# Performance work log

Measured on AMD Instinct MI355X. Metric: run time of the kernel, lower is better.

The kernel has to match this reference:

```python
import jax, jax.numpy as jnp
import numpy as np

THRESHOLD = 0.05

def binarize101(w, threshold):
    # Ternary quantization to {-1, 0, +1}: zero inside the dead-zone [-thr, thr].
    pos = (w > threshold).astype(w.dtype)
    neg = (w < -threshold).astype(w.dtype)
    return pos - neg

def setup_inputs() -> dict:
    key = jax.random.key(0)
    k1, k2, k3 = jax.random.split(key, 3)
    x = jax.random.normal(k1, (8192, 4096), dtype=jnp.float32)
    weight = jax.random.normal(k2, (4096, 4096), dtype=jnp.float32)
    bias = jax.random.normal(k3, (4096,), dtype=jnp.float32)
    return {"x": x, "weight": weight, "bias": bias}

def reference(x, weight, bias):
    wb = binarize101(weight, THRESHOLD)
    # F.linear: x @ wb.T + bias ; x: [N, in], weight: [out, in] -> [N, out]
    return jnp.einsum('ni,oi->no', x, wb) + bias
```

## Files before the change

kernel.cpp:

```cpp
#include <hip/hip_runtime.h>

typedef float floatx4 __attribute__((ext_vector_type(4)));
typedef __bf16 bf16x8 __attribute__((ext_vector_type(8)));
using u16 = unsigned short;
using u32 = unsigned int;

#define GLOBAL_AS __attribute__((address_space(1)))
#define LDS_AS    __attribute__((address_space(3)))

__global__ void cvt_x_kernel(const float* __restrict__ x, u16* __restrict__ xb, int n8) {
  int stride = gridDim.x * blockDim.x;
  for (int i = blockIdx.x * blockDim.x + threadIdx.x; i < n8; i += stride) {
    const float4* p = (const float4*)(x + (size_t)i * 8);
    float4 a = p[0], b = p[1];
    float v[8] = {a.x, a.y, a.z, a.w, b.x, b.y, b.z, b.w};
    u32 r[8];
#pragma unroll
    for (int j = 0; j < 8; ++j) {
      u32 u = __float_as_uint(v[j]);
      r[j] = (u + 0x7FFFu + ((u >> 16) & 1u)) >> 16;
    }
    uint4 o;
    o.x = r[0] | (r[1] << 16);
    o.y = r[2] | (r[3] << 16);
    o.z = r[4] | (r[5] << 16);
    o.w = r[6] | (r[7] << 16);
    *(uint4*)(xb + (size_t)i * 8) = o;
  }
}

__global__ void quant_w_kernel(const float* __restrict__ w, u16* __restrict__ wb, int n8) {
  int stride = gridDim.x * blockDim.x;
  for (int i = blockIdx.x * blockDim.x + threadIdx.x; i < n8; i += stride) {
    const float4* p = (const float4*)(w + (size_t)i * 8);
    float4 a = p[0], b = p[1];
    float v[8] = {a.x, a.y, a.z, a.w, b.x, b.y, b.z, b.w};
    u32 r[8];
#pragma unroll
    for (int j = 0; j < 8; ++j) {
      r[j] = (v[j] > 0.05f) ? 0x3F80u : ((v[j] < -0.05f) ? -1.0f == -1.0f ? 0xBF80u : 0u : 0u);
    }
    uint4 o;
    o.x = r[0] | (r[1] << 16);
    o.y = r[2] | (r[3] << 16);
    o.z = r[4] | (r[5] << 16);
    o.w = r[6] | (r[7] << 16);
    *(uint4*)(wb + (size_t)i * 8) = o;
  }
}

__global__ __launch_bounds__(512, 2) void gemm_bin_pipe(
    const u16* __restrict__ A, const u16* __restrict__ B,
    const float* __restrict__ bias, float* __restrict__ C,
    int M, int N, int K) {
  __shared__ u16 lds[65536];

  const int tid = threadIdx.x;
  const int w = tid >> 6, l = tid & 63;
  const int wr = w >> 2, wc = w & 3;
  const int r = l & 15;

  const int nbn = N >> 8;
  int wg = blockIdx.x;
  const int nwg = gridDim.x;
  if ((nwg & 7) == 0) wg = (wg & 7) * (nwg >> 3) + (wg >> 3);
  const int bm = wg / nbn, bn = wg % nbn;

  const int NSTEPS = K >> 5;

  const int prow = ((tid >> 6) << 4) + (tid & 15);
  const int pk = ((tid >> 4) & 3) << 3;
  const size_t Abase = (size_t)(bm * 256 + prow) * K + pk;
  const size_t Bbase = (size_t)(bn * 256 + prow) * K + pk;
  const size_t chunkStride = (size_t)128 * K;

  const u16* const ldsA = lds + wr * 4096 + l * 8;
  const u16* const ldsB = lds + 8192 + wc * 2048 + l * 8;

  floatx4 acc[8][4] = {};
  bf16x8 afA[8], bfA[4], afB[8], bfB[4];

#define GLOAD(gptr, ldsoff)                                                    \
  __builtin_amdgcn_global_load_lds((const GLOBAL_AS void*)(gptr),              \
                                   (LDS_AS void*)(lds + (ldsoff)), 16, 0, 0)

  for (int u = 0; u < 4; ++u) {
    const int so = u * 16384;
    const u16* ga = A + Abase + (size_t)u * 32;
    const u16* gb = B + Bbase + (size_t)u * 32;
    GLOAD(ga, so + tid * 8);
    GLOAD(ga + chunkStride, so + 4096 + tid * 8);
    GLOAD(gb, so + 8192 + tid * 8);
    GLOAD(gb + chunkStride, so + 12288 + tid * 8);
  }
  asm volatile("s_waitcnt vmcnt(8)" ::: "memory");
  __builtin_amdgcn_s_barrier();
#pragma unroll
  for (int m = 0; m < 8; ++m) afA[m] = *(const bf16x8*)(ldsA + m * 512);
#pragma unroll
  for (int n = 0; n < 4; ++n) bfA[n] = *(const bf16x8*)(ldsB + n * 512);

#define STEP(s, CURA, CURB, NXTA, NXTB)                                        \
  {                                                                            \
    if ((s) >= 1 && (s) + 3 < NSTEPS) {                                        \
      const int sd_ = (((s) + 3) & 3) * 16384;                                 \
      const u16* ga_ = A + Abase + (size_t)((s) + 3) * 32;                     \
      const u16* gb_ = B + Bbase + (size_t)((s) + 3) * 32;                     \
      GLOAD(ga_, sd_ + tid * 8);                                               \
      GLOAD(ga_ + chunkStride, sd_ + 4096 + tid * 8);                          \
      GLOAD(gb_, sd_ + 8192 + tid * 8);                                        \
      GLOAD(gb_ + chunkStride, sd_ + 12288 + tid * 8);                         \
    }                                                                          \
    const int son_ = (((s) + 1) & 3) * 16384;                                  \
    _Pragma("unroll")                                                          \
    for (int m = 0; m < 8; ++m) NXTA[m] = *(const bf16x8*)(ldsA + son_ + m * 512); \
    _Pragma("unroll")                                                          \
    for (int n = 0; n < 4; ++n) NXTB[n] = *(const bf16x8*)(ldsB + son_ + n * 512); \
    asm volatile("s_waitcnt lgkmcnt(12)" ::: "memory");                        \
    __builtin_amdgcn_sched_barrier(0);                                         \
    __builtin_amdgcn_s_setprio(1);                                             \
    _Pragma("unroll")                                                          \
    for (int m = 0; m < 8; ++m)                                                \
      _Pragma("unroll")                                                        \
      for (int n = 0; n < 4; ++n)                                              \
        acc[m][n] = __builtin_amdgcn_mfma_f32_16x16x32_bf16(CURA[m], CURB[n],  \
                                                            acc[m][n], 0, 0, 0); \
    __builtin_amdgcn_s_setprio(0);                                             \
    __builtin_amdgcn_sched_barrier(0);                                         \
    if ((s) + 1 < NSTEPS) {                                                    \
      if ((s) + 3 < NSTEPS) asm volatile("s_waitcnt vmcnt(4)" ::: "memory");   \
      else                  asm volatile("s_waitcnt vmcnt(0)" ::: "memory");   \
      __builtin_amdgcn_s_barrier();                                            \
    }                                                                          \
  }

  for (int t = 0; t < (NSTEPS >> 1); ++t) {
    const int s0 = t << 1;
    STEP(s0,     afA, bfA, afB, bfB);
    STEP(s0 + 1, afB, bfB, afA, bfA);
  }
#undef STEP
#undef GLOAD

  const int g = l >> 4;
  const int colb = bn * 256 + wc * 64;
  float bv[4];
#pragma unroll
  for (int n = 0; n < 4; ++n) bv[n] = bias[colb + n * 16 + r];
  const int rowb0 = bm * 256 + wr * 128;
#pragma unroll
  for (int m = 0; m < 8; ++m) {
    const int rowb = rowb0 + m * 16 + g * 4;
#pragma unroll
    for (int n = 0; n < 4; ++n) {
      const int col = colb + n * 16 + r;
      float* cp = C + (size_t)rowb * N + col;
#pragma unroll
      for (int q = 0; q < 4; ++q) cp[(size_t)q * N] = acc[m][n][q] + bv[n];
    }
  }
}

__global__ void gemm_naive_kernel(const float* __restrict__ x, const float* __restrict__ wgt,
                                  const float* __restrict__ bias, float* __restrict__ out,
                                  int M, int N, int K) {
  long long idx = (long long)blockIdx.x * blockDim.x + threadIdx.x;
  if (idx >= (long long)M * N) return;
  int o = (int)(idx % N);
  int m = (int)(idx / N);
  const float* xr = x + (size_t)m * K;
  const float* wr = wgt + (size_t)o * K;
  float s = 0.f;
  for (int i = 0; i < K; ++i) {
    float wv = wr[i];
    float t = (wv > 0.05f) ? 1.f : ((wv < -0.05f) ? -1.f : 0.f);
    s = fmaf(xr[i], t, s);
  }
  out[idx] = s + bias[o];
}

extern "C" void kernel_launch(void* const* d_in, const int* in_sizes, int n_in,
                              void* d_out, int out_size, void* d_ws, size_t ws_size,
                              hipStream_t stream) {
  const float* x    = (const float*)d_in[0];
  const float* wgt  = (const float*)d_in[1];
  const float* bias = (const float*)d_in[2];
  float* out = (float*)d_out;

  const int N = in_sizes[2];
  const int K = in_sizes[1] / N;
  const int M = in_sizes[0] / K;

  const size_t need = ((size_t)M * K + (size_t)N * K) * sizeof(u16);
  if (ws_size >= need && (M % 256 == 0) && (N % 256 == 0) && (K % 64 == 0) && K >= 256) {
    u16* xb = (u16*)d_ws;
    u16* wb = xb + (size_t)M * K;
    const int nx8 = (M * K) / 8;
    const int nw8 = (N * K) / 8;
    cvt_x_kernel<<<2048, 256, 0, stream>>>(x, xb, nx8);
    quant_w_kernel<<<2048, 256, 0, stream>>>(wgt, wb, nw8);
    const int grid = (M / 256) * (N / 256);
    gemm_bin_pipe<<<grid, 512, 0, stream>>>(xb, wb, bias, out, M, N, K);
  } else {
    const long long total = (long long)M * N;
    gemm_naive_kernel<<<(unsigned)((total + 255) / 256), 256, 0, stream>>>(x, wgt, bias, out, M, N, K);
  }
}
```

Measured before the change: 326.7 us.

## Pre-permute ternary weights into fragment order and load B directly to registers

The weight quantization kernel now writes the bf16 ternary weights in a layout that matches the MFMA fragment order per 256-column tile. The GEMM reads B straight from global memory into registers, keeps only A in LDS (halved LDS, double-buffered with a 64-wide K tile), and splits each tile's MFMAs into quarters with two A fragment reloads. This removes B's LDS traffic and barriers, at the cost of exposed global-load latency on B. Waiting for lgkmcnt(0) before each MFMA batch also reduces overlap.

```diff
diff --git a/kernel.cpp b/kernel.cpp
--- a/kernel.cpp
+++ b/kernel.cpp
@@ -29,31 +29,39 @@
   }
 }
 
-__global__ void quant_w_kernel(const float* __restrict__ w, u16* __restrict__ wb, int n8) {
+__global__ void quant_w_perm(const float* __restrict__ w, u16* __restrict__ wb,
+                             int K, int Kd8, int n8) {
   int stride = gridDim.x * blockDim.x;
   for (int i = blockIdx.x * blockDim.x + threadIdx.x; i < n8; i += stride) {
-    const float4* p = (const float4*)(w + (size_t)i * 8);
+    const int n = i / Kd8;
+    const int k = (i - n * Kd8) * 8;
+    const float4* p = (const float4*)(w + (size_t)n * K + k);
     float4 a = p[0], b = p[1];
     float v[8] = {a.x, a.y, a.z, a.w, b.x, b.y, b.z, b.w};
     u32 r[8];
 #pragma unroll
     for (int j = 0; j < 8; ++j) {
-      r[j] = (v[j] > 0.05f) ? 0x3F80u : ((v[j] < -0.05f) ? -1.0f == -1.0f ? 0xBF80u : 0u : 0u);
+      r[j] = (v[j] > 0.05f) ? 0x3F80u : ((v[j] < -0.05f) ? 0xBF80u : 0u);
     }
     uint4 o;
     o.x = r[0] | (r[1] << 16);
     o.y = r[2] | (r[3] << 16);
     o.z = r[4] | (r[5] << 16);
     o.w = r[6] | (r[7] << 16);
-    *(uint4*)(wb + (size_t)i * 8) = o;
-  }
-}
-
-__global__ __launch_bounds__(512, 2) void gemm_bin_pipe(
-    const u16* __restrict__ A, const u16* __restrict__ B,
+    const int bnp = n >> 8, nl = n & 255;
+    const int wcg = nl >> 6, ng = (nl >> 4) & 3, rr = nl & 15;
+    const int tile = k >> 6, jj = (k >> 5) & 1, g = (k >> 3) & 3;
+    const int f = ng * 2 + jj, l = g * 16 + rr;
+    u16* dst = wb + (size_t)bnp * 256 * K + tile * 16384 + wcg * 4096 + f * 512 + l * 8;
+    *(uint4*)dst = o;
+  }
+}
+
+__global__ __launch_bounds__(512, 2) void gemm_bdir(
+    const u16* __restrict__ A, const u16* __restrict__ Bp,
     const float* __restrict__ bias, float* __restrict__ C,
     int M, int N, int K) {
-  __shared__ u16 lds[65536];
+  __shared__ u16 lds[32768];
 
   const int tid = threadIdx.x;
   const int w = tid >> 6, l = tid & 63;
@@ -66,81 +74,98 @@
   if ((nwg & 7) == 0) wg = (wg & 7) * (nwg >> 3) + (wg >> 3);
   const int bm = wg / nbn, bn = wg % nbn;
 
-  const int NSTEPS = K >> 5;
-
-  const int prow = ((tid >> 6) << 4) + (tid & 15);
-  const int pk = ((tid >> 4) & 3) << 3;
-  const size_t Abase = (size_t)(bm * 256 + prow) * K + pk;
-  const size_t Bbase = (size_t)(bn * 256 + prow) * K + pk;
-  const size_t chunkStride = (size_t)128 * K;
-
-  const u16* const ldsA = lds + wr * 4096 + l * 8;
-  const u16* const ldsB = lds + 8192 + wc * 2048 + l * 8;
+  const int T = K >> 6;
+
+  const u16* Asrc[4];
+#pragma unroll
+  for (int c = 0; c < 4; ++c) {
+    const int e = c * 4096 + tid * 8;
+    const int half = e >> 13, fi = (e >> 9) & 15, ll = (e >> 3) & 63;
+    const int mg = fi >> 1, j = fi & 1, g = ll >> 4, rr2 = ll & 15;
+    const int row = bm * 256 + half * 128 + mg * 16 + rr2;
+    Asrc[c] = A + (size_t)row * K + j * 32 + g * 8;
+  }
+  const u16* const Bbase = Bp + (size_t)bn * 256 * K + wc * 4096 + l * 8;
+  const u16* const ldsA = lds + wr * 8192 + l * 8;
 
   floatx4 acc[8][4] = {};
-  bf16x8 afA[8], bfA[4], afB[8], bfB[4];
-
-#define GLOAD(gptr, ldsoff)                                                    \
-  __builtin_amdgcn_global_load_lds((const GLOBAL_AS void*)(gptr),              \
-                                   (LDS_AS void*)(lds + (ldsoff)), 16, 0, 0)
-
-  for (int u = 0; u < 4; ++u) {
-    const int so = u * 16384;
-    const u16* ga = A + Abase + (size_t)u * 32;
-    const u16* gb = B + Bbase + (size_t)u * 32;
-    GLOAD(ga, so + tid * 8);
-    GLOAD(ga + chunkStride, so + 4096 + tid * 8);
-    GLOAD(gb, so + 8192 + tid * 8);
-    GLOAD(gb + chunkStride, so + 12288 + tid * 8);
-  }
+  bf16x8 af[8], BAs[8], BBs[8];
+
+#define AST(tt, bufoff)                                                        \
+  {                                                                            \
+    _Pragma("unroll")                                                          \
+    for (int c = 0; c < 4; ++c)                                                \
+      __builtin_amdgcn_global_load_lds(                                        \
+          (const GLOBAL_AS void*)(Asrc[c] + (size_t)(tt) * 64),                \
+          (LDS_AS void*)(lds + (bufoff) + c * 4096 + tid * 8), 16, 0, 0);      \
+  }
+#define BLD(tt, DST)                                                           \
+  {                                                                            \
+    _Pragma("unroll")                                                          \
+    for (int f = 0; f < 8; ++f)                                                \
+      DST[f] = *(const bf16x8*)(Bbase + (size_t)(tt) * 16384 + f * 512);       \
+  }
+
+  AST(0, 0);
+  BLD(0, BAs);
   asm volatile("s_waitcnt vmcnt(8)" ::: "memory");
   __builtin_amdgcn_s_barrier();
-#pragma unroll
-  for (int m = 0; m < 8; ++m) afA[m] = *(const bf16x8*)(ldsA + m * 512);
-#pragma unroll
-  for (int n = 0; n < 4; ++n) bfA[n] = *(const bf16x8*)(ldsB + n * 512);
-
-#define STEP(s, CURA, CURB, NXTA, NXTB)                                        \
+
+#define MFMA_Q(MGOFF, NGOFF, CUR)                                              \
+  __builtin_amdgcn_s_setprio(1);                                               \
+  _Pragma("unroll")                                                            \
+  for (int mg = 0; mg < 4; ++mg)                                               \
+    _Pragma("unroll")                                                          \
+    for (int ng = 0; ng < 2; ++ng)                                             \
+      _Pragma("unroll")                                                        \
+      for (int j = 0; j < 2; ++j)                                              \
+        acc[(MGOFF) + mg][(NGOFF) + ng] =                                      \
+            __builtin_amdgcn_mfma_f32_16x16x32_bf16(                           \
+                af[mg * 2 + j], CUR[(NGOFF) * 2 + ng * 2 + j],                 \
+                acc[(MGOFF) + mg][(NGOFF) + ng], 0, 0, 0);                     \
+  __builtin_amdgcn_s_setprio(0);
+
+#define TILE(t, CUR, NXT, DOST)                                                \
   {                                                                            \
-    if ((s) >= 1 && (s) + 3 < NSTEPS) {                                        \
-      const int sd_ = (((s) + 3) & 3) * 16384;                                 \
-      const u16* ga_ = A + Abase + (size_t)((s) + 3) * 32;                     \
-      const u16* gb_ = B + Bbase + (size_t)((s) + 3) * 32;                     \
-      GLOAD(ga_, sd_ + tid * 8);                                               \
-      GLOAD(ga_ + chunkStride, sd_ + 4096 + tid * 8);                          \
-      GLOAD(gb_, sd_ + 8192 + tid * 8);                                        \
-      GLOAD(gb_ + chunkStride, sd_ + 12288 + tid * 8);                         \
+    const int buf_ = ((t) & 1) * 16384;                                        \
+    if (DOST) {                                                                \
+      AST((t) + 1, buf_ ^ 16384);                                              \
+      BLD((t) + 1, NXT);                                                       \
     }                                                                          \
-    const int son_ = (((s) + 1) & 3) * 16384;                                  \
-    _Pragma("unroll")                                                          \
-    for (int m = 0; m < 8; ++m) NXTA[m] = *(const bf16x8*)(ldsA + son_ + m * 512); \
-    _Pragma("unroll")                                                          \
-    for (int n = 0; n < 4; ++n) NXTB[n] = *(const bf16x8*)(ldsB + son_ + n * 512); \
-    asm volatile("s_waitcnt lgkmcnt(12)" ::: "memory");                        \
+                                                   \
+    _Pragma("unroll")                                                          \
+    for (int fi = 0; fi < 8; ++fi)                                             \
+      af[fi] = *(const bf16x8*)(ldsA + buf_ + fi * 512);                       \
+    asm volatile("s_waitcnt lgkmcnt(0)" ::: "memory");                         \
     __builtin_amdgcn_sched_barrier(0);                                         \
-    __builtin_amdgcn_s_setprio(1);                                             \
-    _Pragma("unroll")                                                          \
-    for (int m = 0; m < 8; ++m)                                                \
-      _Pragma("unroll")                                                        \
-      for (int n = 0; n < 4; ++n)                                              \
-        acc[m][n] = __builtin_amdgcn_mfma_f32_16x16x32_bf16(CURA[m], CURB[n],  \
-                                                            acc[m][n], 0, 0, 0); \
-    __builtin_amdgcn_s_setprio(0);                                             \
+    MFMA_Q(0, 0, CUR)                                                          \
+                                                                       \
+    MFMA_Q(0, 2, CUR)                                                          \
+                                                  \
+    _Pragma("unroll")                                                          \
+    for (int fi = 0; fi < 8; ++fi)                                             \
+      af[fi] = *(const bf16x8*)(ldsA + buf_ + 4096 + fi * 512);                \
+    asm volatile("s_waitcnt lgkmcnt(0)" ::: "memory");                         \
     __builtin_amdgcn_sched_barrier(0);                                         \
-    if ((s) + 1 < NSTEPS) {                                                    \
-      if ((s) + 3 < NSTEPS) asm volatile("s_waitcnt vmcnt(4)" ::: "memory");   \
-      else                  asm volatile("s_waitcnt vmcnt(0)" ::: "memory");   \
+    MFMA_Q(4, 0, CUR)                                                          \
+                                                                       \
+    MFMA_Q(4, 2, CUR)                                                          \
+    if (DOST) {                                                                \
+      asm volatile("s_waitcnt vmcnt(8)" ::: "memory");  \
       __builtin_amdgcn_s_barrier();                                            \
     }                                                                          \
   }
 
-  for (int t = 0; t < (NSTEPS >> 1); ++t) {
-    const int s0 = t << 1;
-    STEP(s0,     afA, bfA, afB, bfB);
-    STEP(s0 + 1, afB, bfB, afA, bfA);
-  }
-#undef STEP
-#undef GLOAD
+  for (int t2 = 0; t2 < T - 2; t2 += 2) {
+    TILE(t2,     BAs, BBs, true);
+    TILE(t2 + 1, BBs, BAs, true);
+  }
+  TILE(T - 2, BAs, BBs, true);
+  TILE(T - 1, BBs, BAs, false);
+#undef TILE
+#undef MFMA_Q
+#undef AST
+#undef BLD
 
   const int g = l >> 4;
   const int colb = bn * 256 + wc * 64;
@@ -198,9 +223,9 @@
     const int nx8 = (M * K) / 8;
     const int nw8 = (N * K) / 8;
     cvt_x_kernel<<<2048, 256, 0, stream>>>(x, xb, nx8);
-    quant_w_kernel<<<2048, 256, 0, stream>>>(wgt, wb, nw8);
+    quant_w_perm<<<2048, 256, 0, stream>>>(wgt, wb, K, K / 8, nw8);
     const int grid = (M / 256) * (N / 256);
-    gemm_bin_pipe<<<grid, 512, 0, stream>>>(xb, wb, bias, out, M, N, K);
+    gemm_bdir<<<grid, 512, 0, stream>>>(xb, wb, bias, out, M, N, K);
   } else {
     const long long total = (long long)M * N;
     gemm_naive_kernel<<<(unsigned)((total + 255) / 256), 256, 0, stream>>>(x, wgt, bias, out, M, N, K);
```

After: 366.0 us. +12.1%, slower.

## Pack ternary weights to 2 bits and decode into LDS inside GEMM

Applied to the files above, without the earlier changes.

Weights are quantized into a 2-bit-per-element packed format, pre-swizzled into the per-tile LDS fragment order, so the GEMM reads one-eighth the B bytes of the bf16 version. The GEMM decodes the packed codes to bf16 in registers and writes them to LDS. It also switches to 64-wide K tiles with double buffering and splits each tile into four MFMA quarter-phases with interleaved loads and barriers. This trades B memory bandwidth and the bf16 weight write for extra ALU decode work, more barriers per tile, and a less deeply pipelined A prefetch.

```diff
diff --git a/kernel.cpp b/kernel.cpp
--- a/kernel.cpp
+++ b/kernel.cpp
@@ -29,28 +29,33 @@
   }
 }
 
-__global__ void quant_w_kernel(const float* __restrict__ w, u16* __restrict__ wb, int n8) {
+__global__ void quant_w_pack(const float* __restrict__ w, u16* __restrict__ wb,
+                             int K, int Kd8, int n8) {
   int stride = gridDim.x * blockDim.x;
   for (int i = blockIdx.x * blockDim.x + threadIdx.x; i < n8; i += stride) {
-    const float4* p = (const float4*)(w + (size_t)i * 8);
+    const int n = i / Kd8;
+    const int k = (i - n * Kd8) * 8;
+    const float4* p = (const float4*)(w + (size_t)n * K + k);
     float4 a = p[0], b = p[1];
     float v[8] = {a.x, a.y, a.z, a.w, b.x, b.y, b.z, b.w};
-    u32 r[8];
-#pragma unroll
-    for (int j = 0; j < 8; ++j) {
-      r[j] = (v[j] > 0.05f) ? 0x3F80u : ((v[j] < -0.05f) ? -1.0f == -1.0f ? 0xBF80u : 0u : 0u);
+    u32 pk = 0;
+#pragma unroll
+    for (int e = 0; e < 8; ++e) {
+      u32 c = (v[e] > 0.05f) ? 1u : ((v[e] < -0.05f) ? 3u : 0u);
+      pk |= c << (2 * e);
     }
-    uint4 o;
-    o.x = r[0] | (r[1] << 16);
-    o.y = r[2] | (r[3] << 16);
-    o.z = r[4] | (r[5] << 16);
-    o.w = r[6] | (r[7] << 16);
-    *(uint4*)(wb + (size_t)i * 8) = o;
-  }
-}
-
-__global__ __launch_bounds__(512, 2) void gemm_bin_pipe(
-    const u16* __restrict__ A, const u16* __restrict__ B,
+    const int panel = n >> 8, nl = n & 255;
+    const int wc = nl >> 6, ng = (nl >> 4) & 3, r = nl & 15;
+    const int tile = k >> 6, j = (k >> 5) & 1, g = (k >> 3) & 3;
+    const int f = ng * 2 + j, l = g * 16 + r;
+    const int wf = ((f >> 2) << 4) + (wc << 2) + (f & 3);
+    const int idx = ((wf >> 2) << 8) + (l << 2) + (wf & 3);
+    wb[(size_t)panel * (K >> 6) * 2048 + tile * 2048 + idx] = (u16)pk;
+  }
+}
+
+__global__ __launch_bounds__(512, 2) void gemm_bin_pk(
+    const u16* __restrict__ A, const u16* __restrict__ Bp,
     const float* __restrict__ bias, float* __restrict__ C,
     int M, int N, int K) {
   __shared__ u16 lds[65536];
@@ -66,81 +71,160 @@
   if ((nwg & 7) == 0) wg = (wg & 7) * (nwg >> 3) + (wg >> 3);
   const int bm = wg / nbn, bn = wg % nbn;
 
-  const int NSTEPS = K >> 5;
-
-  const int prow = ((tid >> 6) << 4) + (tid & 15);
-  const int pk = ((tid >> 4) & 3) << 3;
-  const size_t Abase = (size_t)(bm * 256 + prow) * K + pk;
-  const size_t Bbase = (size_t)(bn * 256 + prow) * K + pk;
-  const size_t chunkStride = (size_t)128 * K;
-
-  const u16* const ldsA = lds + wr * 4096 + l * 8;
-  const u16* const ldsB = lds + 8192 + wc * 2048 + l * 8;
+  const int T = K >> 6;
+
+  const int srow = ((tid >> 7) << 4) + (tid & 15);
+  const int skk = (((tid >> 6) & 1) << 5) + (((tid >> 4) & 3) << 3);
+  const size_t aLo0 = (size_t)(bm * 256 + srow) * K + skk;
+  const size_t cs = (size_t)128 * K;
+
+  const u16* const pkp = Bp + (size_t)bn * (K >> 6) * 2048 + ((tid >> 6) << 8) + ((tid & 63) << 2);
+  const int bdst = 16384 + ((tid >> 6) << 11) + ((tid & 63) << 3);
+
+  const u16* const afp0 = lds + wr * 8192 + l * 8;
+  const u16* const bfp0 = lds + 16384 + wc * 2048 + l * 8;
 
   floatx4 acc[8][4] = {};
-  bf16x8 afA[8], bfA[4], afB[8], bfB[4];
-
-#define GLOAD(gptr, ldsoff)                                                    \
+  bf16x8 af[8], bflo[4], bfhi[4];
+  uint2 pkA, pkB;
+
+#define GLOAD(gptr, u16off)                                                    \
   __builtin_amdgcn_global_load_lds((const GLOBAL_AS void*)(gptr),              \
-                                   (LDS_AS void*)(lds + (ldsoff)), 16, 0, 0)
-
-  for (int u = 0; u < 4; ++u) {
-    const int so = u * 16384;
-    const u16* ga = A + Abase + (size_t)u * 32;
-    const u16* gb = B + Bbase + (size_t)u * 32;
-    GLOAD(ga, so + tid * 8);
-    GLOAD(ga + chunkStride, so + 4096 + tid * 8);
-    GLOAD(gb, so + 8192 + tid * 8);
-    GLOAD(gb + chunkStride, so + 12288 + tid * 8);
-  }
-  asm volatile("s_waitcnt vmcnt(8)" ::: "memory");
-  __builtin_amdgcn_s_barrier();
-#pragma unroll
-  for (int m = 0; m < 8; ++m) afA[m] = *(const bf16x8*)(ldsA + m * 512);
-#pragma unroll
-  for (int n = 0; n < 4; ++n) bfA[n] = *(const bf16x8*)(ldsB + n * 512);
-
-#define STEP(s, CURA, CURB, NXTA, NXTB)                                        \
+                                   (LDS_AS void*)(lds + (u16off)), 16, 0, 0)
+#define BARRIER __builtin_amdgcn_s_barrier()
+#define LGKM0  do { asm volatile("s_waitcnt lgkmcnt(0)" ::: "memory");         \
+                    __builtin_amdgcn_sched_barrier(0); } while (0)
+
+#define DECODE(PK, bufn_)                                                      \
   {                                                                            \
-    if ((s) >= 1 && (s) + 3 < NSTEPS) {                                        \
-      const int sd_ = (((s) + 3) & 3) * 16384;                                 \
-      const u16* ga_ = A + Abase + (size_t)((s) + 3) * 32;                     \
-      const u16* gb_ = B + Bbase + (size_t)((s) + 3) * 32;                     \
-      GLOAD(ga_, sd_ + tid * 8);                                               \
-      GLOAD(ga_ + chunkStride, sd_ + 4096 + tid * 8);                          \
-      GLOAD(gb_, sd_ + 8192 + tid * 8);                                        \
-      GLOAD(gb_ + chunkStride, sd_ + 12288 + tid * 8);                         \
+    _Pragma("unroll")                                                          \
+    for (int q = 0; q < 4; ++q) {                                              \
+      u32 word = (q < 2) ? PK.x : PK.y;                                        \
+      u32 vv = (q & 1) ? (word >> 16) : (word & 0xFFFFu);                      \
+      u32 o[4];                                                                \
+      _Pragma("unroll")                                                        \
+      for (int ii = 0; ii < 4; ++ii) {                                         \
+        u32 x = (vv >> (4 * ii)) & 0xFu;                                       \
+        u32 c0 = x & 3u, c1 = x >> 2;                                          \
+        u32 lo = c0 * 0x3F80u + ((c0 >> 1) << 8);                              \
+        u32 hi = c1 * 0x3F80u + ((c1 >> 1) << 8);                              \
+        o[ii] = lo | (hi << 16);                                               \
+      }                                                                        \
+      uint4 ov; ov.x = o[0]; ov.y = o[1]; ov.z = o[2]; ov.w = o[3];            \
+      *(uint4*)(lds + (bufn_) + bdst + q * 512) = ov;                          \
     }                                                                          \
-    const int son_ = (((s) + 1) & 3) * 16384;                                  \
-    _Pragma("unroll")                                                          \
-    for (int m = 0; m < 8; ++m) NXTA[m] = *(const bf16x8*)(ldsA + son_ + m * 512); \
-    _Pragma("unroll")                                                          \
-    for (int n = 0; n < 4; ++n) NXTB[n] = *(const bf16x8*)(ldsB + son_ + n * 512); \
-    asm volatile("s_waitcnt lgkmcnt(12)" ::: "memory");                        \
-    __builtin_amdgcn_sched_barrier(0);                                         \
-    __builtin_amdgcn_s_setprio(1);                                             \
-    _Pragma("unroll")                                                          \
-    for (int m = 0; m < 8; ++m)                                                \
-      _Pragma("unroll")                                                        \
-      for (int n = 0; n < 4; ++n)                                              \
-        acc[m][n] = __builtin_amdgcn_mfma_f32_16x16x32_bf16(CURA[m], CURB[n],  \
-                                                            acc[m][n], 0, 0, 0); \
-    __builtin_amdgcn_s_setprio(0);                                             \
-    __builtin_amdgcn_sched_barrier(0);                                         \
-    if ((s) + 1 < NSTEPS) {                                                    \
-      if ((s) + 3 < NSTEPS) asm volatile("s_waitcnt vmcnt(4)" ::: "memory");   \
-      else                  asm volatile("s_waitcnt vmcnt(0)" ::: "memory");   \
-      __builtin_amdgcn_s_barrier();                                            \
+  }
+
+  pkA = *(const uint2*)(pkp);
+  pkB = *(const uint2*)(pkp + 2048);
+  GLOAD(A + aLo0,                    0 + tid * 8);
+  GLOAD(A + aLo0 + cs,            8192 + tid * 8);
+  GLOAD(A + aLo0 + (size_t)64 * K,        4096 + tid * 8);
+  GLOAD(A + aLo0 + (size_t)64 * K + cs,  12288 + tid * 8);
+  DECODE(pkA, 0)
+  asm volatile("s_waitcnt vmcnt(0)" ::: "memory");
+  asm volatile("s_waitcnt lgkmcnt(0)" ::: "memory");
+  BARRIER;
+
+#define TILE(t, PKC, PKN)                                                      \
+  {                                                                            \
+    const int bufc = ((t) & 1) << 15;                                          \
+    const int bufn = bufc ^ 32768;                                             \
+    const bool doSt = (t) + 1 < T;                                             \
+    const bool doPk = (t) + 2 < T;                                             \
+    const size_t kadv = (size_t)((t) + 1) << 6;                                \
+    const u16* afp = afp0 + bufc;                                              \
+    const u16* bfp = bfp0 + bufc;                                              \
+            \
+    if (doPk) PKN = *(const uint2*)(pkp + (size_t)((t) + 2) * 2048);           \
+    _Pragma("unroll")                                                          \
+    for (int i = 0; i < 8; ++i) af[i] = *(const bf16x8*)(afp + i * 512);       \
+    _Pragma("unroll")                                                          \
+    for (int i = 0; i < 4; ++i) bflo[i] = *(const bf16x8*)(bfp + i * 512);     \
+    if (doSt) {                                                                \
+      GLOAD(A + aLo0 + kadv,      bufn + 0 + tid * 8);                         \
+      GLOAD(A + aLo0 + cs + kadv, bufn + 8192 + tid * 8);                      \
     }                                                                          \
-  }
-
-  for (int t = 0; t < (NSTEPS >> 1); ++t) {
-    const int s0 = t << 1;
-    STEP(s0,     afA, bfA, afB, bfB);
-    STEP(s0 + 1, afB, bfB, afA, bfA);
-  }
-#undef STEP
+    asm volatile("s_waitcnt lgkmcnt(8)" ::: "memory");                         \
+    BARRIER;                                                                   \
+    LGKM0;                                                                     \
+    __builtin_amdgcn_s_setprio(1);                                             \
+    _Pragma("unroll")                                                          \
+    for (int j = 0; j < 2; ++j)                                                \
+      _Pragma("unroll")                                                        \
+      for (int mg = 0; mg < 4; ++mg)                                           \
+        _Pragma("unroll")                                                      \
+        for (int ng = 0; ng < 2; ++ng)                                         \
+          acc[mg][ng] = __builtin_amdgcn_mfma_f32_16x16x32_bf16(               \
+              af[mg * 2 + j], bflo[ng * 2 + j], acc[mg][ng], 0, 0, 0);         \
+    __builtin_amdgcn_s_setprio(0);                                             \
+    BARRIER;                                                                   \
+                 \
+    _Pragma("unroll")                                                          \
+    for (int i = 0; i < 4; ++i) bfhi[i] = *(const bf16x8*)(bfp + 8192 + i * 512); \
+    if (doSt) DECODE(PKC, bufn)                                                \
+    BARRIER;                                                                   \
+    LGKM0;                                                                     \
+    __builtin_amdgcn_s_setprio(1);                                             \
+    _Pragma("unroll")                                                          \
+    for (int j = 0; j < 2; ++j)                                                \
+      _Pragma("unroll")                                                        \
+      for (int mg = 0; mg < 4; ++mg)                                           \
+        _Pragma("unroll")                                                      \
+        for (int ng = 0; ng < 2; ++ng)                                         \
+          acc[mg][2 + ng] = __builtin_amdgcn_mfma_f32_16x16x32_bf16(           \
+              af[mg * 2 + j], bfhi[ng * 2 + j], acc[mg][2 + ng], 0, 0, 0);     \
+    __builtin_amdgcn_s_setprio(0);                                             \
+    if (doPk) asm volatile("s_waitcnt vmcnt(3)" ::: "memory");                 \
+    else      asm volatile("s_waitcnt vmcnt(0)" ::: "memory");                 \
+    BARRIER;                                                                   \
+                                       \
+    _Pragma("unroll")                                                          \
+    for (int i = 0; i < 8; ++i) af[i] = *(const bf16x8*)(afp + 4096 + i * 512); \
+    asm volatile("s_waitcnt lgkmcnt(4)" ::: "memory");                         \
+    BARRIER;                                                                   \
+    LGKM0;                                                                     \
+    __builtin_amdgcn_s_setprio(1);                                             \
+    _Pragma("unroll")                                                          \
+    for (int j = 0; j < 2; ++j)                                                \
+      _Pragma("unroll")                                                        \
+      for (int mg = 0; mg < 4; ++mg)                                           \
+        _Pragma("unroll")                                                      \
+        for (int ng = 0; ng < 2; ++ng)                                         \
+          acc[4 + mg][ng] = __builtin_amdgcn_mfma_f32_16x16x32_bf16(           \
+              af[mg * 2 + j], bflo[ng * 2 + j], acc[4 + mg][ng], 0, 0, 0);     \
+    __builtin_amdgcn_s_setprio(0);                                             \
+    BARRIER;                                                                   \
+                                     \
+    if (doSt) {                                                                \
+      GLOAD(A + aLo0 + (size_t)64 * K + kadv,      bufn + 4096 + tid * 8);     \
+      GLOAD(A + aLo0 + (size_t)64 * K + cs + kadv, bufn + 12288 + tid * 8);    \
+    }                                                                          \
+    BARRIER;                                                                   \
+    __builtin_amdgcn_s_setprio(1);                                             \
+    _Pragma("unroll")                                                          \
+    for (int j = 0; j < 2; ++j)                                                \
+      _Pragma("unroll")                                                        \
+      for (int mg = 0; mg < 4; ++mg)                                           \
+        _Pragma("unroll")                                                      \
+        for (int ng = 0; ng < 2; ++ng)                                         \
+          acc[4 + mg][2 + ng] = __builtin_amdgcn_mfma_f32_16x16x32_bf16(       \
+              af[mg * 2 + j], bfhi[ng * 2 + j], acc[4 + mg][2 + ng], 0, 0, 0); \
+    __builtin_amdgcn_s_setprio(0);                                             \
+    if (doPk) asm volatile("s_waitcnt vmcnt(2)" ::: "memory");                 \
+    else      asm volatile("s_waitcnt vmcnt(0)" ::: "memory");                 \
+    BARRIER;                                                                   \
+  }
+
+  for (int tt = 0; tt < T; tt += 2) {
+    TILE(tt,     pkB, pkA)
+    TILE(tt + 1, pkA, pkB)
+  }
+#undef TILE
+#undef DECODE
 #undef GLOAD
+#undef BARRIER
+#undef LGKM0
 
   const int g = l >> 4;
   const int colb = bn * 256 + wc * 64;
@@ -191,16 +275,16 @@
   const int K = in_sizes[1] / N;
   const int M = in_sizes[0] / K;
 
-  const size_t need = ((size_t)M * K + (size_t)N * K) * sizeof(u16);
-  if (ws_size >= need && (M % 256 == 0) && (N % 256 == 0) && (K % 64 == 0) && K >= 256) {
+  const size_t need = (size_t)M * K * 2 + (size_t)N * K / 4;
+  if (ws_size >= need && (M % 256 == 0) && (N % 256 == 0) && (K % 128 == 0) && K >= 256) {
     u16* xb = (u16*)d_ws;
     u16* wb = xb + (size_t)M * K;
     const int nx8 = (M * K) / 8;
     const int nw8 = (N * K) / 8;
     cvt_x_kernel<<<2048, 256, 0, stream>>>(x, xb, nx8);
-    quant_w_kernel<<<2048, 256, 0, stream>>>(wgt, wb, nw8);
+    quant_w_pack<<<2048, 256, 0, stream>>>(wgt, wb, K, K / 8, nw8);
     const int grid = (M / 256) * (N / 256);
-    gemm_bin_pipe<<<grid, 512, 0, stream>>>(xb, wb, bias, out, M, N, K);
+    gemm_bin_pk<<<grid, 512, 0, stream>>>(xb, wb, bias, out, M, N, K);
   } else {
     const long long total = (long long)M * N;
     gemm_naive_kernel<<<(unsigned)((total + 255) / 256), 256, 0, stream>>>(x, wgt, bias, out, M, N, K);
```

Result: slower. 378.1 us (+15.7%).
